# Kernel optimization log

Hardware: AMD Instinct MI355X
Metric: run time of the kernel (lower is better)

## Reference

```python
import jax, jax.numpy as jnp
import numpy as np

B, C, L = 16, 512, 8192
K = 7  # kernel_size, symmetric padding K//2 = 3


def setup_inputs() -> dict:
    key = jax.random.key(0)
    k1, k2, k3 = jax.random.split(key, 3)
    x = jax.random.normal(k1, (B, C, L), dtype=jnp.float32)
    mask = jax.random.randint(k2, (B, 1, L), 0, 2).astype(bool)
    # Conv1d(2 -> 1, kernel 7, no bias): weight shape (out=1, in=2, k=7)
    conv_w = jax.random.normal(k3, (1, 2, K), dtype=jnp.float32) * (1.0 / np.sqrt(2 * K))
    return {"x": x, "mask": mask, "conv_w": conv_w}


def reference(x, mask, conv_w):
    # Channel-wise max and mean pooling -> (B, 1, L) each
    max_c = jnp.max(x, axis=1, keepdims=True)
    avg_c = jnp.mean(x, axis=1, keepdims=True)
    # NOTE: in the original torch code, every masked_fill_ call uses the
    # out-of-place masked_fill and its return value is discarded, so the mask
    # has NO effect on the computation. We replicate that faithfully: `mask`
    # is accepted but unused.
    feats = jnp.concatenate([max_c, avg_c], axis=1)  # (B, 2, L)
    logits = jax.lax.conv_general_dilated(
        feats, conv_w,
        window_strides=(1,),
        padding=[(K // 2, K // 2)],
        dimension_numbers=("NCH", "OIH", "NCH"),
    )  # (B, 1, L)
    attn = jax.nn.sigmoid(logits)
    return attn * x  # (B, C, L)
```

## Files before the change

kernel.cpp:

```cpp
#include <hip/hip_runtime.h>
#include <math.h>

#define NB 16
#define NC 512
#define NL 8192
#define KW 7

__global__ __launch_bounds__(256) void sam1d_pool(
    const float* __restrict__ x, float* __restrict__ feats) {
    const int gid = blockIdx.x * 256 + threadIdx.x;
    const int b = gid / NL;
    const int l = gid - b * NL;

    const float* p = x + (size_t)b * NC * NL + l;
    float mx = -INFINITY;
    float sm = 0.0f;
#pragma unroll 8
    for (int c = 0; c < NC; ++c) {
        float v = p[(size_t)c * NL];
        mx = fmaxf(mx, v);
        sm += v;
    }
    float* f = feats + (size_t)b * 2 * NL;
    f[l]      = mx;
    f[NL + l] = sm * (1.0f / (float)NC);
}

__global__ __launch_bounds__(256) void sam1d_apply(
    const float* __restrict__ x, const float* __restrict__ feats,
    const float* __restrict__ w, float* __restrict__ out) {
    const int gid = blockIdx.x * 256 + threadIdx.x;
    const int b = gid / NL;
    const int l = gid - b * NL;

    const float* fm = feats + (size_t)b * 2 * NL;
    const float* fa = fm + NL;

    float logit = 0.0f;
#pragma unroll
    for (int k = 0; k < KW; ++k) {
        int ll = l + k - (KW / 2);
        if (ll >= 0 && ll < NL) {
            logit = fmaf(fm[ll], w[k], logit);
            logit = fmaf(fa[ll], w[KW + k], logit);
        }
    }
    const float attn = 1.0f / (1.0f + expf(-logit));

    const float* px = x + (size_t)b * NC * NL + l;
    float* po = out + (size_t)b * NC * NL + l;
#pragma unroll 8
    for (int c = 0; c < NC; ++c) {
        po[(size_t)c * NL] = attn * px[(size_t)c * NL];
    }
}

extern "C" void kernel_launch(void* const* d_in, const int* in_sizes, int n_in,
                              void* d_out, int out_size, void* d_ws, size_t ws_size,
                              hipStream_t stream) {
    const float* x = (const float*)d_in[0];
    const float* w = (const float*)d_in[2];
    float* out = (float*)d_out;
    float* feats = (float*)d_ws;

    const int total = NB * NL;
    const int blocks = total / 256;

    sam1d_pool<<<blocks, 256, 0, stream>>>(x, feats);
    sam1d_apply<<<blocks, 256, 0, stream>>>(x, feats, w, out);
}
```

Before: 167.5 us.

## Fuse pooling and attention apply into one kernel with register-cached tiles

Merges the channel pooling and the conv+sigmoid+scale kernels into a single kernel. Each block loads a 64-column tile (with a 3-column halo) across all channels into registers, reduces max/mean through LDS, computes the conv and sigmoid locally, then writes the output from the cached values. This removes the second full read of x and the feats workspace round trip. In exchange, halo columns are loaded redundantly, accesses are unaligned to the tile stride, and register pressure per thread is higher.

Result: faster. 164.2 us (-2.0%).

```diff
diff --git a/kernel.cpp b/kernel.cpp
--- a/kernel.cpp
+++ b/kernel.cpp
@@ -6,52 +6,75 @@
 #define NL 8192
 #define KW 7
 
-__global__ __launch_bounds__(256) void sam1d_pool(
-    const float* __restrict__ x, float* __restrict__ feats) {
-    const int gid = blockIdx.x * 256 + threadIdx.x;
-    const int b = gid / NL;
-    const int l = gid - b * NL;
+#define TILE 64
+#define HALO (KW / 2)
+#define TIN  (TILE - 2 * HALO)
+#define NTILES ((NL + TIN - 1) / TIN)
+#define CG  16
+#define CPT (NC / CG)
 
-    const float* p = x + (size_t)b * NC * NL + l;
-    float mx = -INFINITY;
-    float sm = 0.0f;
-#pragma unroll 8
-    for (int c = 0; c < NC; ++c) {
-        float v = p[(size_t)c * NL];
-        mx = fmaxf(mx, v);
-        sm += v;
+__global__ __launch_bounds__(1024) void sam1d_fused(
+    const float* __restrict__ x, const float* __restrict__ w,
+    float* __restrict__ out) {
+    __shared__ float lds_mx[CG * TILE];
+    __shared__ float lds_sm[CG * TILE];
+    __shared__ float pool_mx[TILE];
+    __shared__ float pool_av[TILE];
+
+    const int tid  = threadIdx.x;
+    const int lcol = tid & (TILE - 1);
+    const int cg   = tid >> 6;
+    const int blk  = blockIdx.x;
+    const int b    = blk / NTILES;
+    const int t    = blk - b * NTILES;
+    const int l    = t * TIN - HALO + lcol;
+    const bool lvalid = (l >= 0) && (l < NL);
+
+    const float* px = x + (size_t)b * NC * NL + (size_t)(cg * CPT) * NL + l;
+
+    float xv[CPT];
+    if (lvalid) {
+#pragma unroll
+        for (int j = 0; j < CPT; ++j) xv[j] = px[(size_t)j * NL];
+    } else {
+#pragma unroll
+        for (int j = 0; j < CPT; ++j) xv[j] = 0.0f;
     }
-    float* f = feats + (size_t)b * 2 * NL;
-    f[l]      = mx;
-    f[NL + l] = sm * (1.0f / (float)NC);
-}
 
-__global__ __launch_bounds__(256) void sam1d_apply(
-    const float* __restrict__ x, const float* __restrict__ feats,
-    const float* __restrict__ w, float* __restrict__ out) {
-    const int gid = blockIdx.x * 256 + threadIdx.x;
-    const int b = gid / NL;
-    const int l = gid - b * NL;
+    float mx = xv[0], sm = xv[0];
+#pragma unroll
+    for (int j = 1; j < CPT; ++j) { mx = fmaxf(mx, xv[j]); sm += xv[j]; }
+    lds_mx[cg * TILE + lcol] = mx;
+    lds_sm[cg * TILE + lcol] = sm;
+    __syncthreads();
 
-    const float* fm = feats + (size_t)b * 2 * NL;
-    const float* fa = fm + NL;
+    if (tid < TILE) {
+        float m = lds_mx[tid];
+#pragma unroll
+        for (int g = 1; g < CG; ++g) m = fmaxf(m, lds_mx[g * TILE + tid]);
+        const int gl = t * TIN - HALO + tid;
+        pool_mx[tid] = (gl >= 0 && gl < NL) ? m : 0.0f;
+    } else if (tid < 2 * TILE) {
+        const int c = tid - TILE;
+        float s = lds_sm[c];
+#pragma unroll
+        for (int g = 1; g < CG; ++g) s += lds_sm[g * TILE + c];
+        const int gl = t * TIN - HALO + c;
+        pool_av[c] = (gl >= 0 && gl < NL) ? s * (1.0f / (float)NC) : 0.0f;
+    }
+    __syncthreads();
 
-    float logit = 0.0f;
+    if (lcol >= HALO && lcol < HALO + TIN && l < NL) {
+        float logit = 0.0f;
 #pragma unroll
-    for (int k = 0; k < KW; ++k) {
-        int ll = l + k - (KW / 2);
-        if (ll >= 0 && ll < NL) {
-            logit = fmaf(fm[ll], w[k], logit);
-            logit = fmaf(fa[ll], w[KW + k], logit);
+        for (int k = 0; k < KW; ++k) {
+            logit = fmaf(pool_mx[lcol - HALO + k], w[k],      logit);
+            logit = fmaf(pool_av[lcol - HALO + k], w[KW + k], logit);
         }
-    }
-    const float attn = 1.0f / (1.0f + expf(-logit));
-
-    const float* px = x + (size_t)b * NC * NL + l;
-    float* po = out + (size_t)b * NC * NL + l;
-#pragma unroll 8
-    for (int c = 0; c < NC; ++c) {
-        po[(size_t)c * NL] = attn * px[(size_t)c * NL];
+        const float attn = 1.0f / (1.0f + expf(-logit));
+        float* po = out + (size_t)b * NC * NL + (size_t)(cg * CPT) * NL + l;
+#pragma unroll
+        for (int j = 0; j < CPT; ++j) po[(size_t)j * NL] = attn * xv[j];
     }
 }
 
@@ -61,11 +84,7 @@
     const float* x = (const float*)d_in[0];
     const float* w = (const float*)d_in[2];
     float* out = (float*)d_out;
-    float* feats = (float*)d_ws;
 
-    const int total = NB * NL;
-    const int blocks = total / 256;
-
-    sam1d_pool<<<blocks, 256, 0, stream>>>(x, feats);
-    sam1d_apply<<<blocks, 256, 0, stream>>>(x, feats, w, out);
+    const int blocks = NB * NTILES;
+    sam1d_fused<<<blocks, 1024, 0, stream>>>(x, w, out);
 }
```

## Split pooling into channel slabs, separate conv stage, vectorized apply kernel

Applied to the files above, without the earlier changes.

Restructures the pipeline into three kernels. Channel reduction is split into 16 slabs per batch, each handled by a 1024-thread block using float4 loads, and writes partial max/sum buffers. A small conv kernel combines the partials, stages them in shared memory and computes the sigmoid attention map. A grid-stride float4 kernel then applies the attention to x. The goal is more parallelism and wider memory transactions, at the cost of an extra launch and an extra partial-buffer round trip.

After: 161.6 us. 3.5% less time.

```diff
diff --git a/kernel.cpp b/kernel.cpp
--- a/kernel.cpp
+++ b/kernel.cpp
@@ -5,53 +5,102 @@
 #define NC 512
 #define NL 8192
 #define KW 7
+#define NF4 (NL / 4)
+#define SLABS 16
+#define SCH (NC / SLABS)
 
-__global__ __launch_bounds__(256) void sam1d_pool(
-    const float* __restrict__ x, float* __restrict__ feats) {
-    const int gid = blockIdx.x * 256 + threadIdx.x;
-    const int b = gid / NL;
-    const int l = gid - b * NL;
+__global__ __launch_bounds__(1024) void k1_pool(
+    const float* __restrict__ x, float* __restrict__ part) {
+    const int blk = blockIdx.x;
+    const int b   = blk >> 4;
+    const int s   = blk & (SLABS - 1);
+    const int tid = threadIdx.x;
 
-    const float* p = x + (size_t)b * NC * NL + l;
-    float mx = -INFINITY;
-    float sm = 0.0f;
-#pragma unroll 8
-    for (int c = 0; c < NC; ++c) {
-        float v = p[(size_t)c * NL];
-        mx = fmaxf(mx, v);
-        sm += v;
+    const float* px = x + (size_t)(b * NC + s * SCH) * NL;
+
+    float4 v0 = *(const float4*)(px + 4 * tid);
+    float4 v1 = *(const float4*)(px + 4 * (tid + 1024));
+    float4 mx0 = v0, sm0 = v0, mx1 = v1, sm1 = v1;
+
+#pragma unroll 4
+    for (int c = 1; c < SCH; ++c) {
+        const float* pr = px + (size_t)c * NL;
+        float4 a = *(const float4*)(pr + 4 * tid);
+        float4 bq = *(const float4*)(pr + 4 * (tid + 1024));
+        mx0.x = fmaxf(mx0.x, a.x);  sm0.x += a.x;
+        mx0.y = fmaxf(mx0.y, a.y);  sm0.y += a.y;
+        mx0.z = fmaxf(mx0.z, a.z);  sm0.z += a.z;
+        mx0.w = fmaxf(mx0.w, a.w);  sm0.w += a.w;
+        mx1.x = fmaxf(mx1.x, bq.x); sm1.x += bq.x;
+        mx1.y = fmaxf(mx1.y, bq.y); sm1.y += bq.y;
+        mx1.z = fmaxf(mx1.z, bq.z); sm1.z += bq.z;
+        mx1.w = fmaxf(mx1.w, bq.w); sm1.w += bq.w;
     }
-    float* f = feats + (size_t)b * 2 * NL;
-    f[l]      = mx;
-    f[NL + l] = sm * (1.0f / (float)NC);
+
+    float* pm = part + ((size_t)blk * 2 + 0) * NL;
+    float* ps = part + ((size_t)blk * 2 + 1) * NL;
+    *(float4*)(pm + 4 * tid)          = mx0;
+    *(float4*)(pm + 4 * (tid + 1024)) = mx1;
+    *(float4*)(ps + 4 * tid)          = sm0;
+    *(float4*)(ps + 4 * (tid + 1024)) = sm1;
 }
 
-__global__ __launch_bounds__(256) void sam1d_apply(
-    const float* __restrict__ x, const float* __restrict__ feats,
-    const float* __restrict__ w, float* __restrict__ out) {
-    const int gid = blockIdx.x * 256 + threadIdx.x;
-    const int b = gid / NL;
-    const int l = gid - b * NL;
+#define K2OUT 250
+__global__ __launch_bounds__(256) void k2_conv(
+    const float* __restrict__ part, const float* __restrict__ w,
+    float* __restrict__ attn) {
+    __shared__ float pm[256], pa[256], wl[2 * KW];
+    const int nt   = (NL + K2OUT - 1) / K2OUT;
+    const int b    = blockIdx.x / nt;
+    const int t    = blockIdx.x - b * nt;
+    const int base = t * K2OUT;
+    const int tid  = threadIdx.x;
+    if (tid < 2 * KW) wl[tid] = w[tid];
 
-    const float* fm = feats + (size_t)b * 2 * NL;
-    const float* fa = fm + NL;
+    const int pc = base - 3 + tid;
+    if (pc >= 0 && pc < NL) {
+        float m = -INFINITY, sm = 0.0f;
+#pragma unroll
+        for (int s = 0; s < SLABS; ++s) {
+            m  = fmaxf(m, part[(((size_t)b * SLABS + s) * 2 + 0) * NL + pc]);
+            sm += part[(((size_t)b * SLABS + s) * 2 + 1) * NL + pc];
+        }
+        pm[tid] = m;
+        pa[tid] = sm * (1.0f / (float)NC);
+    } else {
+        pm[tid] = 0.0f;
+        pa[tid] = 0.0f;
+    }
+    __syncthreads();
 
-    float logit = 0.0f;
+    const int l = base + tid;
+    if (tid < K2OUT && l < NL) {
+        float logit = 0.0f;
 #pragma unroll
-    for (int k = 0; k < KW; ++k) {
-        int ll = l + k - (KW / 2);
-        if (ll >= 0 && ll < NL) {
-            logit = fmaf(fm[ll], w[k], logit);
-            logit = fmaf(fa[ll], w[KW + k], logit);
+        for (int k = 0; k < KW; ++k) {
+            logit = fmaf(pm[tid + k], wl[k],      logit);
+            logit = fmaf(pa[tid + k], wl[KW + k], logit);
         }
+        attn[(size_t)b * NL + l] = 1.0f / (1.0f + expf(-logit));
     }
-    const float attn = 1.0f / (1.0f + expf(-logit));
+}
 
-    const float* px = x + (size_t)b * NC * NL + l;
-    float* po = out + (size_t)b * NC * NL + l;
-#pragma unroll 8
-    for (int c = 0; c < NC; ++c) {
-        po[(size_t)c * NL] = attn * px[(size_t)c * NL];
+__global__ __launch_bounds__(256) void k3_apply(
+    const float* __restrict__ x, const float* __restrict__ attn,
+    float* __restrict__ out) {
+    const size_t total  = (size_t)NB * NC * NF4;
+    const size_t stride = (size_t)gridDim.x * 256;
+    for (size_t i = (size_t)blockIdx.x * 256 + threadIdx.x; i < total; i += stride) {
+        const int col4 = (int)(i & (NF4 - 1));
+        const int b    = (int)(i >> 20);
+        float4 xv = *(const float4*)(x + 4 * i);
+        float4 at = *(const float4*)(attn + ((size_t)b << 13) + 4 * (size_t)col4);
+        float4 o;
+        o.x = at.x * xv.x;
+        o.y = at.y * xv.y;
+        o.z = at.z * xv.z;
+        o.w = at.w * xv.w;
+        *(float4*)(out + 4 * i) = o;
     }
 }
 
@@ -61,11 +110,11 @@
     const float* x = (const float*)d_in[0];
     const float* w = (const float*)d_in[2];
     float* out = (float*)d_out;
-    float* feats = (float*)d_ws;
 
-    const int total = NB * NL;
-    const int blocks = total / 256;
+    float* part = (float*)d_ws;
+    float* attn = part + (size_t)NB * SLABS * 2 * NL;
 
-    sam1d_pool<<<blocks, 256, 0, stream>>>(x, feats);
-    sam1d_apply<<<blocks, 256, 0, stream>>>(x, feats, w, out);
+    k1_pool<<<NB * SLABS, 1024, 0, stream>>>(x, part);
+    k2_conv<<<NB * ((NL + K2OUT - 1) / K2OUT), 256, 0, stream>>>(part, w, attn);
+    k3_apply<<<2048, 256, 0, stream>>>(x, attn, out);
 }
```
